# Optimization experiments

Hardware: AMD Instinct MI355X
Metric: run time of the kernel (lower is better)

The kernel has to match this reference:

```python
import jax, jax.numpy as jnp
import numpy as np
import math

B, S, D = 2, 1024, 1024
H, KVH = 16, 4
HD = D // H            # 64
WIN = 256              # sliding window size
E, TOPK = 8, 2
DFF = 4096
T = B * S
CAP = max(1, int(1.0 * T / E))   # capacity_factor=1.0 -> 256
EPS = 1e-6
NEG_INF = float('-inf')


def setup_inputs() -> dict:
    key = jax.random.key(0)
    ks = jax.random.split(key, 10)
    x = jax.random.normal(ks[0], (B, S, D), dtype=jnp.float32)
    # causal additive mask (B,1,S,S)
    i = jnp.arange(S)[:, None]
    j = jnp.arange(S)[None, :]
    causal = jnp.where(j <= i, 0.0, NEG_INF).astype(jnp.float32)
    mask = jnp.broadcast_to(causal[None, None], (B, 1, S, S))
    global_token_mask = jax.random.uniform(ks[1], (B, S)) < 0.05
    sd = 1.0 / math.sqrt(D)
    Wq = jax.random.normal(ks[2], (D, D), jnp.float32) * sd
    Wk = jax.random.normal(ks[3], (D, D), jnp.float32) * sd
    Wv = jax.random.normal(ks[4], (D, D), jnp.float32) * sd
    Wo = jax.random.normal(ks[5], (D, D), jnp.float32) * sd
    g1 = jnp.ones((D,), jnp.float32)
    g2 = jnp.ones((D,), jnp.float32)
    Wgate = jax.random.normal(ks[6], (D, E), jnp.float32) * 0.02
    W1 = jax.random.normal(ks[7], (E, D, 2 * DFF), jnp.float32) * sd
    W2 = jax.random.normal(ks[8], (E, DFF, D), jnp.float32) * (1.0 / math.sqrt(DFF))
    return {"x": x, "mask": mask, "global_token_mask": global_token_mask,
            "Wq": Wq, "Wk": Wk, "Wv": Wv, "Wo": Wo,
            "g1": g1, "g2": g2, "Wgate": Wgate, "W1": W1, "W2": W2}


def _rope_tables():
    inv_freq = 1.0 / (10000.0 ** (jnp.arange(0, HD, 2, dtype=jnp.float32) / HD))
    t = jnp.arange(S, dtype=jnp.float32)
    freqs = t[:, None] * inv_freq[None, :]          # (S, HD/2)
    emb = jnp.concatenate([freqs, freqs], axis=-1)  # (S, HD)
    return emb[None, None].astype(jnp.float32), None  # placeholder


def _rotate_half(x):
    x1, x2 = jnp.split(x, 2, axis=-1)
    return jnp.concatenate([-x2, x1], axis=-1)


def _rmsnorm(x, g):
    return g * x * jax.lax.rsqrt(jnp.mean(x * x, axis=-1, keepdims=True) + EPS)


def _attention(x, mask, gtm, Wq, Wk, Wv, Wo):
    # The torch GQA view/permute chain reduces exactly to a plain head split.
    q = (x @ Wq).reshape(B, S, H, HD).transpose(0, 2, 1, 3)  # (B,H,S,HD)
    k = (x @ Wk).reshape(B, S, H, HD).transpose(0, 2, 1, 3)
    v = (x @ Wv).reshape(B, S, H, HD).transpose(0, 2, 1, 3)
    # inline RoPE
    inv_freq = 1.0 / (10000.0 ** (jnp.arange(0, HD, 2, dtype=jnp.float32) / HD))
    t = jnp.arange(S, dtype=jnp.float32)
    freqs = t[:, None] * inv_freq[None, :]
    emb = jnp.concatenate([freqs, freqs], axis=-1)  # (S,HD)
    cos = jnp.cos(emb)[None, None]
    sin = jnp.sin(emb)[None, None]
    q = q * cos + _rotate_half(q) * sin
    k = k * cos + _rotate_half(k) * sin
    scores = jnp.einsum('bhqd,bhkd->bhqk', q, k) / math.sqrt(HD)
    # sliding-window mask
    i = jnp.arange(S)[:, None]
    j = jnp.arange(S)[None, :]
    diff = i - j
    swa = jnp.where((diff < 0) | (diff >= WIN), NEG_INF, 0.0).astype(scores.dtype)
    combined = mask + swa[None, None]               # (B,1,S,S)
    gt = gtm[:, None, :, None]                      # query is global
    gs = gtm[:, None, None, :]                      # key is global
    combined = jnp.where(gt | gs, 0.0, combined)
    attn = jax.nn.softmax(scores + combined, axis=-1)
    out = jnp.einsum('bhqk,bhkd->bhqd', attn, v)
    out = out.transpose(0, 2, 1, 3).reshape(B, S, D)
    return out @ Wo


def _moe(x, Wgate, W1, W2):
    flat_x = x.reshape(T, D)
    gate_scores = jax.nn.softmax(flat_x @ Wgate, axis=-1)          # (T,E)
    topk_vals, topk_idx = jax.lax.top_k(gate_scores, TOPK)          # (T,k)
    phi_mean = jnp.mean(gate_scores, axis=0)
    aux_loss = E * jnp.sum(phi_mean * phi_mean)
    # per-token weight for each expert (0 if not routed)
    w = jnp.zeros((T, E), flat_x.dtype).at[jnp.arange(T)[:, None], topk_idx].add(topk_vals)
    # capacity: pick top-CAP tokens by weight per expert. Unrouted tokens have
    # weight 0 so any that slip in contribute exactly 0 (matches torch semantics).
    sel_w, sel_idx = jax.lax.top_k(w.T, CAP)                        # (E,CAP)
    tok = flat_x[sel_idx]                                           # (E,CAP,D)
    h = jnp.einsum('ecd,edf->ecf', tok, W1)                         # (E,CAP,2*DFF)
    h1, h2 = jnp.split(h, 2, axis=-1)
    act = h1 * jax.nn.silu(h2)                                      # SwiGLU
    out_e = jnp.einsum('ecf,efd->ecd', act, W2) * sel_w[..., None]
    combined = jnp.zeros((T, D), flat_x.dtype).at[sel_idx.reshape(-1)].add(out_e.reshape(-1, D))
    return combined.reshape(B, S, D), aux_loss


def reference(x, mask, global_token_mask, Wq, Wk, Wv, Wo, g1, g2, Wgate, W1, W2):
    # pre-norm residual block (SublayerConnection with RMSNorm, dropout=identity in eval)
    h = x + _attention(_rmsnorm(x, g1), mask, global_token_mask, Wq, Wk, Wv, Wo)
    moe_out, aux_loss = _moe(_rmsnorm(h, g2), Wgate, W1, W2)
    out = h + moe_out
    return out, aux_loss
```

## Files before the change

### kernel.cpp

```cpp
#include <hip/hip_runtime.h>
#include <hip/hip_bf16.h>
#include <math.h>

#define T_TOK 2048
#define DMODEL 1024
#define NH 16
#define HD 64
#define S_LEN 1024
#define NE 8
#define CAP 256
#define DFF 4096

typedef __attribute__((ext_vector_type(8))) short bf16x8;
typedef __attribute__((ext_vector_type(4))) float f32x4;

__device__ inline unsigned short f2bf(float f) {
    union { float f; unsigned int u; } x; x.f = f;
    unsigned int u = x.u;
    unsigned int r = (u + 0x7FFFu + ((u >> 16) & 1u)) >> 16;
    return (unsigned short)r;
}

__device__ inline float bf2f(unsigned short h) {
    union { unsigned int u; float f; } x; x.u = (unsigned int)h << 16; return x.f;
}

__device__ inline unsigned int pkbf(float lo, float hi) {
    __hip_bfloat162 h2 = __float22bfloat162_rn(make_float2(lo, hi));
    unsigned int r;
    __builtin_memcpy(&r, &h2, 4);
    return r;
}

__device__ inline void gload16(const void* g, void* l) {
    __builtin_amdgcn_global_load_lds(
        (const __attribute__((address_space(1))) unsigned int*)g,
        (__attribute__((address_space(3))) unsigned int*)l, 16, 0, 0);
}

__global__ void rope_table_kernel(float* __restrict__ rc, float* __restrict__ rs) {
    int s = blockIdx.x;
    int i = threadIdx.x;
    float invf = powf(10000.0f, -(float)(2 * i) / 64.0f);
    float ang = (float)s * invf;
    rc[s * 32 + i] = cosf(ang);
    rs[s * 32 + i] = sinf(ang);
}

template <int OUTBF>
__global__ __launch_bounds__(256) void rmsnorm_kernel(const float* __restrict__ x,
                                                      const float* __restrict__ g,
                                                      void* __restrict__ yv) {
    __shared__ float red[256];
    int t = blockIdx.x;
    int tid = threadIdx.x;
    const float* xr = x + (size_t)t * DMODEL;
    float ss = 0.f;
    for (int d = tid; d < DMODEL; d += 256) { float v = xr[d]; ss += v * v; }
    red[tid] = ss; __syncthreads();
    for (int o = 128; o > 0; o >>= 1) { if (tid < o) red[tid] += red[tid + o]; __syncthreads(); }
    float scale = 1.0f / sqrtf(red[0] / (float)DMODEL + 1e-6f);
    if (OUTBF) {
        unsigned short* yr = (unsigned short*)yv + (size_t)t * DMODEL;
        for (int d = tid; d < DMODEL; d += 256) yr[d] = f2bf(g[d] * xr[d] * scale);
    } else {
        float* yr = (float*)yv + (size_t)t * DMODEL;
        for (int d = tid; d < DMODEL; d += 256) yr[d] = g[d] * xr[d] * scale;
    }
}

__global__ __launch_bounds__(256) void transpose_bf16(const float* __restrict__ src,
                                                      unsigned short* __restrict__ dst,
                                                      int ldS, int ldD,
                                                      long long sS, long long sD) {
    __shared__ float tile[64][65];
    src += (long long)blockIdx.z * sS;
    dst += (long long)blockIdx.z * sD;
    int c0 = blockIdx.x * 64, r0 = blockIdx.y * 64;
    int tr = threadIdx.x >> 4;
    int tc4 = (threadIdx.x & 15) * 4;
    #pragma unroll
    for (int j = 0; j < 4; j++) {
        float4 v = *(const float4*)&src[(size_t)(r0 + tr + j * 16) * ldS + c0 + tc4];
        tile[tr + j * 16][tc4 + 0] = v.x;
        tile[tr + j * 16][tc4 + 1] = v.y;
        tile[tr + j * 16][tc4 + 2] = v.z;
        tile[tr + j * 16][tc4 + 3] = v.w;
    }
    __syncthreads();
    int oc = threadIdx.x >> 3;
    int or8 = (threadIdx.x & 7) * 8;
    #pragma unroll
    for (int j = 0; j < 2; j++) {
        int c = oc + j * 32;
        unsigned short tmp[8];
        #pragma unroll
        for (int u = 0; u < 8; u++) tmp[u] = f2bf(tile[or8 + u][c]);
        *(uint4*)&dst[(size_t)(c0 + c) * ldD + r0 + or8] = *(uint4*)tmp;
    }
}

template <int BN, int RES>
__global__ __launch_bounds__(256) void gemm_mfma(const unsigned short* __restrict__ A,
                                                 const unsigned short* __restrict__ BT,
                                                 const float* __restrict__ Rr,
                                                 float* __restrict__ C,
                                                 int K, int lda, int ldc,
                                                 long long sA, long long sB, long long sC) {
    constexpr int BM = 128, BK = 64;
    constexpr int NF = BN / 32;
    __shared__ unsigned short As[BM * BK];
    __shared__ unsigned short Bs[BN * BK];
    A += (long long)blockIdx.z * sA;
    BT += (long long)blockIdx.z * sB;
    C += (long long)blockIdx.z * sC;
    const int tid = threadIdx.x;
    const int lane = tid & 63;
    const int wid = tid >> 6;
    const int wr = wid >> 1, wc = wid & 1;
    const int bx = blockIdx.x * BN, by = blockIdx.y * BM;

    f32x4 acc[4][NF] = {};

    for (int k0 = 0; k0 < K; k0 += BK) {
        #pragma unroll
        for (int i = 0; i < (BM * 8) / 256; i++) {
            int c = i * 256 + tid;
            int row = c >> 3, slot = c & 7;
            int gs = slot ^ (row & 7);
            gload16(A + (size_t)(by + row) * lda + k0 + gs * 8, &As[c * 8]);
        }
        #pragma unroll
        for (int i = 0; i < (BN * 8) / 256; i++) {
            int c = i * 256 + tid;
            int row = c >> 3, slot = c & 7;
            int gs = slot ^ (row & 7);
            gload16(BT + (size_t)(bx + row) * K + k0 + gs * 8, &Bs[c * 8]);
        }
        __syncthreads();
        #pragma unroll
        for (int ks = 0; ks < 2; ks++) {
            bf16x8 af[4], bfr[NF];
            #pragma unroll
            for (int m = 0; m < 4; m++) {
                int row = wr * 64 + m * 16 + (lane & 15);
                int slot = (ks * 4 + (lane >> 4)) ^ (row & 7);
                af[m] = *(const bf16x8*)&As[row * 64 + slot * 8];
            }
            #pragma unroll
            for (int n = 0; n < NF; n++) {
                int row = wc * (BN / 2) + n * 16 + (lane & 15);
                int slot = (ks * 4 + (lane >> 4)) ^ (row & 7);
                bfr[n] = *(const bf16x8*)&Bs[row * 64 + slot * 8];
            }
            #pragma unroll
            for (int m = 0; m < 4; m++)
                #pragma unroll
                for (int n = 0; n < NF; n++)
                    acc[m][n] = __builtin_amdgcn_mfma_f32_16x16x32_bf16(af[m], bfr[n], acc[m][n], 0, 0, 0);
        }
        __syncthreads();
    }
    #pragma unroll
    for (int m = 0; m < 4; m++) {
        int row0 = by + wr * 64 + m * 16 + (lane >> 4) * 4;
        #pragma unroll
        for (int n = 0; n < NF; n++) {
            int col = bx + wc * (BN / 2) + n * 16 + (lane & 15);
            #pragma unroll
            for (int r = 0; r < 4; r++) {
                size_t idx = (size_t)(row0 + r) * ldc + col;
                float v = acc[m][n][r];
                if (RES == 1) v += Rr[idx];
                if (RES == 2) v += C[idx];
                C[idx] = v;
            }
        }
    }
}

__global__ __launch_bounds__(256) void gemm_w1_fused(const unsigned short* __restrict__ tok,
                                                     const float* __restrict__ W1,
                                                     unsigned short* __restrict__ act) {
    __shared__ unsigned short As[256 * 64];
    __shared__ unsigned int B1p[32 * 32];
    __shared__ unsigned int B2p[32 * 32];
    const int e = blockIdx.y;
    const int bx = blockIdx.x * 32;
    const unsigned short* A = tok + (size_t)e * CAP * DMODEL;
    const float* B = W1 + (size_t)e * DMODEL * (2 * DFF);
    unsigned short* C = act + (size_t)e * CAP * DFF;
    const int tid = threadIdx.x, l = tid & 63, wid = tid >> 6;
    const int g = l >> 4;
    const int kp = tid >> 3;
    const int nc = tid & 7;
    const int chunk = kp >> 2, within = kp & 3;

    f32x4 acc1[4][2] = {};
    f32x4 acc2[4][2] = {};

    for (int k0 = 0; k0 < DMODEL; k0 += 64) {
        #pragma unroll
        for (int i = 0; i < 8; i++) {
            int c = i * 256 + tid;
            int row = c >> 3, sl = c & 7, gs = sl ^ (row & 7);
            gload16(A + (size_t)row * DMODEL + k0 + gs * 8, &As[c * 8]);
        }
        const float* Brow = B + (size_t)(k0 + 2 * kp) * 8192 + bx + nc * 4;
        float4 a0 = *(const float4*)(Brow);
        float4 a1 = *(const float4*)(Brow + 8192);
        float4 c0 = *(const float4*)(Brow + 4096);
        float4 c1 = *(const float4*)(Brow + 4096 + 8192);
        unsigned int p1[4], p2[4];
        p1[0] = pkbf(a0.x, a1.x); p1[1] = pkbf(a0.y, a1.y);
        p1[2] = pkbf(a0.z, a1.z); p1[3] = pkbf(a0.w, a1.w);
        p2[0] = pkbf(c0.x, c1.x); p2[1] = pkbf(c0.y, c1.y);
        p2[2] = pkbf(c0.z, c1.z); p2[3] = pkbf(c0.w, c1.w);
        #pragma unroll
        for (int i = 0; i < 4; i++) {
            int n_loc = nc * 4 + i;
            int idx = n_loc * 32 + ((chunk ^ (n_loc & 7)) << 2) + within;
            B1p[idx] = p1[i];
            B2p[idx] = p2[i];
        }
        __syncthreads();
        #pragma unroll
        for (int ks = 0; ks < 2; ks++) {
            bf16x8 af[4];
            #pragma unroll
            for (int m = 0; m < 4; m++) {
                int row = wid * 64 + m * 16 + (l & 15);
                int sl = (ks * 4 + g) ^ (row & 7);
                af[m] = *(const bf16x8*)&As[row * 64 + sl * 8];
            }
            #pragma unroll
            for (int nf = 0; nf < 2; nf++) {
                int n_loc = nf * 16 + (l & 15);
                int base = n_loc * 32 + (((ks * 4 + g) ^ (n_loc & 7)) << 2);
                bf16x8 b1 = *(const bf16x8*)&B1p[base];
                bf16x8 b2 = *(const bf16x8*)&B2p[base];
                #pragma unroll
                for (int m = 0; m < 4; m++) {
                    acc1[m][nf] = __builtin_amdgcn_mfma_f32_16x16x32_bf16(af[m], b1, acc1[m][nf], 0, 0, 0);
                    acc2[m][nf] = __builtin_amdgcn_mfma_f32_16x16x32_bf16(af[m], b2, acc2[m][nf], 0, 0, 0);
                }
            }
        }
        __syncthreads();
    }
    #pragma unroll
    for (int m = 0; m < 4; m++) {
        int row0 = wid * 64 + m * 16 + (l >> 4) * 4;
        #pragma unroll
        for (int nf = 0; nf < 2; nf++) {
            int col = bx + nf * 16 + (l & 15);
            #pragma unroll
            for (int r = 0; r < 4; r++) {
                float h1 = acc1[m][nf][r], h2 = acc2[m][nf][r];
                float sil = h2 / (1.0f + __expf(-h2));
                C[(size_t)(row0 + r) * DFF + col] = f2bf(h1 * sil);
            }
        }
    }
}

__global__ __launch_bounds__(256) void gemm_w2_fused(const unsigned short* __restrict__ act,
                                                     const float* __restrict__ W2,
                                                     float* __restrict__ oute) {
    __shared__ unsigned short As[128 * 64];
    __shared__ unsigned int Bp[32 * 32];
    const int e = blockIdx.y >> 1, mb = blockIdx.y & 1;
    const int bx = blockIdx.x * 32;
    const unsigned short* A = act + (size_t)e * CAP * DFF + (size_t)mb * 128 * DFF;
    const float* B = W2 + (size_t)e * DFF * DMODEL;
    float* C = oute + (size_t)e * CAP * DMODEL + (size_t)mb * 128 * DMODEL;
    const int tid = threadIdx.x, l = tid & 63, wid = tid >> 6;
    const int g = l >> 4;
    const int kp = tid >> 3;
    const int nc = tid & 7;
    const int chunk = kp >> 2, within = kp & 3;

    f32x4 acc[2][2] = {};

    for (int k0 = 0; k0 < DFF; k0 += 64) {
        #pragma unroll
        for (int i = 0; i < 4; i++) {
            int c = i * 256 + tid;
            int row = c >> 3, sl = c & 7, gs = sl ^ (row & 7);
            gload16(A + (size_t)row * DFF + k0 + gs * 8, &As[c * 8]);
        }
        const float* Brow = B + (size_t)(k0 + 2 * kp) * DMODEL + bx + nc * 4;
        float4 a0 = *(const float4*)(Brow);
        float4 a1 = *(const float4*)(Brow + DMODEL);
        unsigned int p1[4];
        p1[0] = pkbf(a0.x, a1.x); p1[1] = pkbf(a0.y, a1.y);
        p1[2] = pkbf(a0.z, a1.z); p1[3] = pkbf(a0.w, a1.w);
        #pragma unroll
        for (int i = 0; i < 4; i++) {
            int n_loc = nc * 4 + i;
            int idx = n_loc * 32 + ((chunk ^ (n_loc & 7)) << 2) + within;
            Bp[idx] = p1[i];
        }
        __syncthreads();
        #pragma unroll
        for (int ks = 0; ks < 2; ks++) {
            bf16x8 af[2];
            #pragma unroll
            for (int m = 0; m < 2; m++) {
                int row = wid * 32 + m * 16 + (l & 15);
                int sl = (ks * 4 + g) ^ (row & 7);
                af[m] = *(const bf16x8*)&As[row * 64 + sl * 8];
            }
            #pragma unroll
            for (int nf = 0; nf < 2; nf++) {
                int n_loc = nf * 16 + (l & 15);
                int base = n_loc * 32 + (((ks * 4 + g) ^ (n_loc & 7)) << 2);
                bf16x8 bfr = *(const bf16x8*)&Bp[base];
                #pragma unroll
                for (int m = 0; m < 2; m++)
                    acc[m][nf] = __builtin_amdgcn_mfma_f32_16x16x32_bf16(af[m], bfr, acc[m][nf], 0, 0, 0);
            }
        }
        __syncthreads();
    }
    #pragma unroll
    for (int m = 0; m < 2; m++) {
        int row0 = wid * 32 + m * 16 + (l >> 4) * 4;
        #pragma unroll
        for (int nf = 0; nf < 2; nf++) {
            int col = bx + nf * 16 + (l & 15);
            #pragma unroll
            for (int r = 0; r < 4; r++)
                C[(size_t)(row0 + r) * DMODEL + col] = acc[m][nf][r];
        }
    }
}

__global__ __launch_bounds__(512) void rope_cvt_kernel(const float* __restrict__ qkv,
                                                       const float* __restrict__ rc,
                                                       const float* __restrict__ rs,
                                                       unsigned short* __restrict__ Qh,
                                                       unsigned short* __restrict__ Ql,
                                                       unsigned short* __restrict__ Kh,
                                                       unsigned short* __restrict__ Kl) {
    int t = blockIdx.x;
    int b = t >> 10, s = t & 1023;
    int hh = threadIdx.x >> 5, i = threadIdx.x & 31;
    float c = rc[s * 32 + i], sn = rs[s * 32 + i];
    size_t base = (size_t)t * 3072 + hh * 64;
    float qa = qkv[base + i], qb_ = qkv[base + i + 32];
    float ka = qkv[base + 1024 + i], kb_ = qkv[base + 1024 + i + 32];
    size_t ob = ((size_t)(b * 16 + hh) * 1024 + s) * 64;
    float q0 = (qa * c - qb_ * sn) * 0.125f;
    float q1 = (qb_ * c + qa * sn) * 0.125f;
    float k0 = ka * c - kb_ * sn;
    float k1 = kb_ * c + ka * sn;
    unsigned short h0, h1;
    h0 = f2bf(q0); Qh[ob + i] = h0;      Ql[ob + i] = f2bf(q0 - bf2f(h0));
    h1 = f2bf(q1); Qh[ob + i + 32] = h1; Ql[ob + i + 32] = f2bf(q1 - bf2f(h1));
    h0 = f2bf(k0); Kh[ob + i] = h0;      Kl[ob + i] = f2bf(k0 - bf2f(h0));
    h1 = f2bf(k1); Kh[ob + i + 32] = h1; Kl[ob + i + 32] = f2bf(k1 - bf2f(h1));
}

__global__ __launch_bounds__(256) void vt_cvt_kernel(const float* __restrict__ qkv,
                                                     unsigned short* __restrict__ Vtb) {
    __shared__ float tile[32][65];
    int st = blockIdx.x;
    int bh = blockIdx.y;
    int b = bh >> 4, h = bh & 15;
    int tid = threadIdx.x;
    int s0 = st * 32;
    int sr = tid >> 3, c8 = (tid & 7) * 8;
    const float* src = qkv + (size_t)(b * 1024 + s0 + sr) * 3072 + 2048 + h * 64 + c8;
    #pragma unroll
    for (int u = 0; u < 8; u++) tile[sr][c8 + u] = src[u];
    __syncthreads();
    int d = tid & 63, sj = (tid >> 6) * 8;
    unsigned short tmp[8];
    #pragma unroll
    for (int u = 0; u < 8; u++) tmp[u] = f2bf(tile[sj + u][d]);
    *(uint4*)(Vtb + ((size_t)bh * 64 + d) * 1024 + s0 + sj) = *(uint4*)tmp;
}

__global__ __launch_bounds__(256) void attn_mfma_kernel(const unsigned short* __restrict__ Qh,
                                                        const unsigned short* __restrict__ Ql,
                                                        const unsigned short* __restrict__ Kh,
                                                        const unsigned short* __restrict__ Kl,
                                                        const unsigned short* __restrict__ Vtb,
                                                        const int* __restrict__ gtm,
                                                        unsigned short* __restrict__ o) {
    __shared__ unsigned short Ksh[64 * 64];
    __shared__ unsigned short Ksl[64 * 64];
    __shared__ unsigned short Vs[64 * 64];
    __shared__ unsigned short Pl[4][16 * 64];
    const int qt = blockIdx.x, h = blockIdx.y, b = blockIdx.z;
    const int bh = b * 16 + h;
    const int tid = threadIdx.x, l = tid & 63, w = tid >> 6;
    const int q0 = qt * 64 + w * 16;
    const unsigned short* Qhb = Qh + (size_t)bh * 1024 * 64;
    const unsigned short* Qlb = Ql + (size_t)bh * 1024 * 64;
    const unsigned short* Khb = Kh + (size_t)bh * 1024 * 64;
    const unsigned short* Klb = Kl + (size_t)bh * 1024 * 64;
    const unsigned short* Vbh = Vtb + (size_t)bh * 64 * 1024;
    const int* gb = gtm + b * 1024;

    bf16x8 afh[2], afl[2];
    #pragma unroll
    for (int ks = 0; ks < 2; ks++) {
        size_t off = (size_t)(q0 + (l & 15)) * 64 + ks * 32 + (l >> 4) * 8;
        afh[ks] = *(const bf16x8*)(Qhb + off);
        afl[ks] = *(const bf16x8*)(Qlb + off);
    }

    int gqm = 0;
    #pragma unroll
    for (int r = 0; r < 4; r++)
        gqm |= (gb[q0 + (l >> 4) * 4 + r] ? 1 : 0) << r;

    f32x4 acc_o[4] = {};
    float m_run[4], l_run[4];
    #pragma unroll
    for (int r = 0; r < 4; r++) { m_run[r] = -1e30f; l_run[r] = 0.f; }

    for (int jt = 0; jt < 16; jt++) {
        const int j0 = jt * 64;
        #pragma unroll
        for (int i = 0; i < 2; i++) {
            int c = i * 256 + tid, row = c >> 3, sl = c & 7, gs = sl ^ (row & 7);
            gload16(Khb + (size_t)(j0 + row) * 64 + gs * 8, &Ksh[c * 8]);
            gload16(Klb + (size_t)(j0 + row) * 64 + gs * 8, &Ksl[c * 8]);
            gload16(Vbh + (size_t)row * 1024 + j0 + gs * 8, &Vs[c * 8]);
        }
        __syncthreads();

        f32x4 sv[4] = {};
        #pragma unroll
        for (int n = 0; n < 4; n++) {
            #pragma unroll
            for (int ks = 0; ks < 2; ks++) {
                int row = n * 16 + (l & 15);
                int sl = (ks * 4 + (l >> 4)) ^ (row & 7);
                bf16x8 khf = *(const bf16x8*)&Ksh[row * 64 + sl * 8];
                bf16x8 klf = *(const bf16x8*)&Ksl[row * 64 + sl * 8];
                sv[n] = __builtin_amdgcn_mfma_f32_16x16x32_bf16(afl[ks], khf, sv[n], 0, 0, 0);
                sv[n] = __builtin_amdgcn_mfma_f32_16x16x32_bf16(afh[ks], klf, sv[n], 0, 0, 0);
                sv[n] = __builtin_amdgcn_mfma_f32_16x16x32_bf16(afh[ks], khf, sv[n], 0, 0, 0);
            }
        }

        int gk[4];
        #pragma unroll
        for (int n = 0; n < 4; n++) gk[n] = gb[j0 + n * 16 + (l & 15)];

        #pragma unroll
        for (int n = 0; n < 4; n++)
            #pragma unroll
            for (int r = 0; r < 4; r++) {
                int q = q0 + (l >> 4) * 4 + r;
                int k = j0 + n * 16 + (l & 15);
                bool allowed = ((gqm >> r) & 1) || gk[n] || ((k <= q) && (q - k < 256));
                if (!allowed) sv[n][r] = -1e30f;
            }

        {
            float tm[4], corr[4], rsum[4];
            #pragma unroll
            for (int r = 0; r < 4; r++)
                tm[r] = fmaxf(fmaxf(sv[0][r], sv[1][r]), fmaxf(sv[2][r], sv[3][r]));
            #pragma unroll
            for (int wd = 1; wd <= 8; wd <<= 1)
                #pragma unroll
                for (int r = 0; r < 4; r++) tm[r] = fmaxf(tm[r], __shfl_xor(tm[r], wd, 64));
            #pragma unroll
            for (int r = 0; r < 4; r++) {
                float mn = fmaxf(m_run[r], tm[r]);
                corr[r] = __expf(m_run[r] - mn);
                m_run[r] = mn;
                rsum[r] = 0.f;
            }
            #pragma unroll
            for (int n = 0; n < 4; n++)
                #pragma unroll
                for (int r = 0; r < 4; r++) {
                    float p = __expf(sv[n][r] - m_run[r]);
                    sv[n][r] = p;
                    rsum[r] += p;
                }
            #pragma unroll
            for (int wd = 1; wd <= 8; wd <<= 1)
                #pragma unroll
                for (int r = 0; r < 4; r++) rsum[r] += __shfl_xor(rsum[r], wd, 64);
            #pragma unroll
            for (int r = 0; r < 4; r++) l_run[r] = l_run[r] * corr[r] + rsum[r];
            #pragma unroll
            for (int nd = 0; nd < 4; nd++)
                #pragma unroll
                for (int r = 0; r < 4; r++) acc_o[nd][r] *= corr[r];
            #pragma unroll
            for (int n = 0; n < 4; n++)
                #pragma unroll
                for (int r = 0; r < 4; r++) {
                    int qr = (l >> 4) * 4 + r;
                    int kc = n * 16 + (l & 15);
                    int byte = (qr * 128 + kc * 2) ^ ((qr & 7) << 4);
                    Pl[w][byte >> 1] = f2bf(sv[n][r]);
                }
        }

        asm volatile("s_waitcnt lgkmcnt(0)" ::: "memory");
        __builtin_amdgcn_sched_barrier(0);

        #pragma unroll
        for (int ks = 0; ks < 2; ks++) {
            int prow = l & 15;
            int psl = (ks * 4 + (l >> 4)) ^ (prow & 7);
            bf16x8 pa = *(const bf16x8*)&Pl[w][prow * 64 + psl * 8];
            #pragma unroll
            for (int nd = 0; nd < 4; nd++) {
                int row = nd * 16 + (l & 15);
                int sl = (ks * 4 + (l >> 4)) ^ (row & 7);
                bf16x8 vf = *(const bf16x8*)&Vs[row * 64 + sl * 8];
                acc_o[nd] = __builtin_amdgcn_mfma_f32_16x16x32_bf16(pa, vf, acc_o[nd], 0, 0, 0);
            }
        }
        __syncthreads();
    }

    #pragma unroll
    for (int r = 0; r < 4; r++) {
        float inv = 1.0f / l_run[r];
        int t_ = b * 1024 + q0 + (l >> 4) * 4 + r;
        #pragma unroll
        for (int nd = 0; nd < 4; nd++) {
            int col = h * 64 + nd * 16 + (l & 15);
            o[(size_t)t_ * 1024 + col] = f2bf(acc_o[nd][r] * inv);
        }
    }
}

__global__ __launch_bounds__(256) void gate_kernel(const float* __restrict__ hn,
                                                   const float* __restrict__ Wgate,
                                                   float* __restrict__ wfull,
                                                   float* __restrict__ gate_sum) {
    int tid = threadIdx.x;
    int w = tid >> 6, l = tid & 63;
    int t = blockIdx.x * 4 + w;
    int e = l & 7, g = l >> 3;
    const float* xr = hn + (size_t)t * DMODEL;
    const float* wp = Wgate + l;
    float acc = 0.f;
    #pragma unroll 8
    for (int kk = 0; kk < 128; kk++)
        acc += xr[g + 8 * kk] * wp[64 * kk];
    #pragma unroll
    for (int o = 8; o < 64; o <<= 1) acc += __shfl_xor(acc, o, 64);
    float m = acc;
    #pragma unroll
    for (int o = 1; o < 8; o <<= 1) m = fmaxf(m, __shfl_xor(m, o, 64));
    float p = __expf(acc - m);
    float s = p;
    #pragma unroll
    for (int o = 1; o < 8; o <<= 1) s += __shfl_xor(s, o, 64);
    float pr = p / s;
    if (l < 8) atomicAdd(&gate_sum[e], pr);
    unsigned long long key = ((unsigned long long)__float_as_uint(pr) << 32) | (unsigned)(7 - e);
    unsigned long long k1 = key;
    #pragma unroll
    for (int o = 1; o < 8; o <<= 1) { unsigned long long t2 = __shfl_xor(k1, o, 64); if (t2 > k1) k1 = t2; }
    int e1 = 7 - (int)(k1 & 7);
    float v1 = __uint_as_float((unsigned)(k1 >> 32));
    unsigned long long key2 = (e == e1) ? 0ull : key;
    unsigned long long k2 = key2;
    #pragma unroll
    for (int o = 1; o < 8; o <<= 1) { unsigned long long t2 = __shfl_xor(k2, o, 64); if (t2 > k2) k2 = t2; }
    int e2 = 7 - (int)(k2 & 7);
    float v2 = __uint_as_float((unsigned)(k2 >> 32));
    if (l == 0) {
        wfull[t * 8 + e1] = v1;
        wfull[t * 8 + e2] = v2;
    }
}

__global__ __launch_bounds__(1024) void expert_select_kernel(const float* __restrict__ wfull,
                                                             float* __restrict__ sw,
                                                             int* __restrict__ sidx,
                                                             int* __restrict__ slot) {
    __shared__ unsigned long long keys[2048];
    int e = blockIdx.x;
    int t = threadIdx.x;
    for (int i = t; i < 2048; i += 1024) {
        float w = wfull[i * 8 + e];
        unsigned int wb = __float_as_uint(w);
        keys[i] = ((unsigned long long)wb << 32) | (unsigned long long)(0xFFFFFFFFu - (unsigned int)i);
    }
    __syncthreads();
    for (int k = 2; k <= 2048; k <<= 1) {
        for (int j = k >> 1; j > 0; j >>= 1) {
            for (int i = t; i < 2048; i += 1024) {
                int ixj = i ^ j;
                if (ixj > i) {
                    bool desc = ((i & k) == 0);
                    unsigned long long a = keys[i], b = keys[ixj];
                    if ((a < b) == desc) { keys[i] = b; keys[ixj] = a; }
                }
            }
            __syncthreads();
        }
    }
    if (t < CAP) {
        unsigned long long kk = keys[t];
        float w = __uint_as_float((unsigned int)(kk >> 32));
        int idx = (int)(0xFFFFFFFFu - (unsigned int)(kk & 0xFFFFFFFFu));
        sw[e * CAP + t] = w;
        sidx[e * CAP + t] = idx;
        if (w > 0.f) slot[idx * 8 + e] = t;
    }
}

__global__ __launch_bounds__(256) void gather_tok_kernel(const float* __restrict__ hn,
                                                         const int* __restrict__ sidx,
                                                         const float* __restrict__ sw,
                                                         unsigned short* __restrict__ tok) {
    int ec = blockIdx.x;
    int tid = threadIdx.x;
    float w = sw[ec];
    int src = sidx[ec];
    const float* s = hn + (size_t)src * DMODEL;
    unsigned short* d = tok + (size_t)ec * DMODEL;
    for (int i = tid; i < DMODEL; i += 256) d[i] = (w > 0.f) ? f2bf(s[i]) : 0;
}

__global__ __launch_bounds__(256) void combine_kernel(const float* __restrict__ h,
                                                      const float* __restrict__ out_e,
                                                      const int* __restrict__ slot,
                                                      const float* __restrict__ wfull,
                                                      const float* __restrict__ gate_sum,
                                                      float* __restrict__ out) {
    int t = blockIdx.x;
    int tid = threadIdx.x;
    for (int d = tid; d < DMODEL; d += 256) {
        float acc = h[(size_t)t * DMODEL + d];
        #pragma unroll
        for (int e = 0; e < 8; e++) {
            int c = slot[t * 8 + e];
            if (c >= 0) acc += wfull[t * 8 + e] * out_e[((size_t)(e * CAP + c)) * DMODEL + d];
        }
        out[(size_t)t * DMODEL + d] = acc;
    }
    if (t == 0 && tid == 0) {
        float a = 0.f;
        #pragma unroll
        for (int e = 0; e < 8; e++) { float m = gate_sum[e] / (float)T_TOK; a += m * m; }
        out[(size_t)T_TOK * DMODEL] = 8.0f * a;
    }
}

extern "C" void kernel_launch(void* const* d_in, const int* in_sizes, int n_in,
                              void* d_out, int out_size, void* d_ws, size_t ws_size,
                              hipStream_t stream) {
    const float* x     = (const float*)d_in[0];
    const int*   gtm   = (const int*)d_in[2];
    const float* Wq    = (const float*)d_in[3];
    const float* Wk    = (const float*)d_in[4];
    const float* Wv    = (const float*)d_in[5];
    const float* Wo    = (const float*)d_in[6];
    const float* g1    = (const float*)d_in[7];
    const float* g2    = (const float*)d_in[8];
    const float* Wgate = (const float*)d_in[9];
    const float* W1    = (const float*)d_in[10];
    const float* W2    = (const float*)d_in[11];
    float* out = (float*)d_out;

    char* ws = (char*)d_ws;
    unsigned short* Qh   = (unsigned short*)(ws + 0);
    unsigned short* Ql   = (unsigned short*)(ws + 4194304);
    unsigned short* Kh   = (unsigned short*)(ws + 8388608);
    unsigned short* Kl   = (unsigned short*)(ws + 12582912);
    unsigned short* Vtb  = (unsigned short*)(ws + 16777216);
    unsigned short* WqkvT = (unsigned short*)(ws + 33554432);
    unsigned short* WoT   = (unsigned short*)(ws + 39845888);
    unsigned short* xn    = (unsigned short*)(ws + 41943040);
    unsigned short* attno = (unsigned short*)(ws + 46137344);
    float* qkvb  = (float*)(ws + 50331648);
    float* oute  = (float*)(ws + 50331648);
    unsigned short* act = (unsigned short*)(ws + 33554432);
    float* hb    = (float*)(ws + 75497472);
    float* hnb   = (float*)(ws + 83886080);
    unsigned short* tok = (unsigned short*)(ws + 92274688);
    float* ropec = (float*)(ws + 96468992);
    float* ropes = (float*)(ws + 96600064);
    float* wfull = (float*)(ws + 96731136);
    int*   slot  = (int*)(ws + 96796672);
    float* sw    = (float*)(ws + 96862208);
    int*   sidx  = (int*)(ws + 96870400);
    float* gsum  = (float*)(ws + 96878592);

    rope_table_kernel<<<S_LEN, 32, 0, stream>>>(ropec, ropes);
    rmsnorm_kernel<1><<<T_TOK, 256, 0, stream>>>(x, g1, xn);

    transpose_bf16<<<dim3(16, 16, 1), 256, 0, stream>>>(Wq, WqkvT, 1024, 1024, 0, 0);
    transpose_bf16<<<dim3(16, 16, 1), 256, 0, stream>>>(Wk, WqkvT + 1024 * 1024, 1024, 1024, 0, 0);
    transpose_bf16<<<dim3(16, 16, 1), 256, 0, stream>>>(Wv, WqkvT + 2048 * 1024, 1024, 1024, 0, 0);
    transpose_bf16<<<dim3(16, 16, 1), 256, 0, stream>>>(Wo, WoT, 1024, 1024, 0, 0);

    gemm_mfma<128, 0><<<dim3(24, 16, 1), 256, 0, stream>>>(
        xn, WqkvT, nullptr, qkvb, 1024, 1024, 3072, 0, 0, 0);

    rope_cvt_kernel<<<T_TOK, 512, 0, stream>>>(qkvb, ropec, ropes, Qh, Ql, Kh, Kl);
    vt_cvt_kernel<<<dim3(32, 32, 1), 256, 0, stream>>>(qkvb, Vtb);

    attn_mfma_kernel<<<dim3(16, 16, 2), 256, 0, stream>>>(Qh, Ql, Kh, Kl, Vtb, gtm, attno);

    gemm_mfma<64, 1><<<dim3(16, 16, 1), 256, 0, stream>>>(
        attno, WoT, x, hb, 1024, 1024, 1024, 0, 0, 0);
    rmsnorm_kernel<0><<<T_TOK, 256, 0, stream>>>(hb, g2, hnb);

    hipMemsetAsync(wfull, 0, (size_t)T_TOK * NE * 4, stream);
    hipMemsetAsync(slot, 0xFF, (size_t)T_TOK * NE * 4, stream);
    hipMemsetAsync(gsum, 0, 8 * 4, stream);

    gate_kernel<<<T_TOK / 4, 256, 0, stream>>>(hnb, Wgate, wfull, gsum);
    expert_select_kernel<<<NE, 1024, 0, stream>>>(wfull, sw, sidx, slot);
    gather_tok_kernel<<<NE * CAP, 256, 0, stream>>>(hnb, sidx, sw, tok);

    gemm_w1_fused<<<dim3(128, 8, 1), 256, 0, stream>>>(tok, W1, act);
    gemm_w2_fused<<<dim3(32, 16, 1), 256, 0, stream>>>(act, W2, oute);

    combine_kernel<<<T_TOK, 256, 0, stream>>>(hb, oute, slot, wfull, gsum, out);
}
```

Before: 372.3 us.

## Fuse QKV projection with RoPE/V-transpose and drop weight transpose and memset launches

After: 356.4 us (median of 2 runs). 1.04x faster.

```diff
diff --git a/kernel.cpp b/kernel.cpp
--- a/kernel.cpp
+++ b/kernel.cpp
@@ -38,13 +38,15 @@
         (__attribute__((address_space(3))) unsigned int*)l, 16, 0, 0);
 }
 
-__global__ void rope_table_kernel(float* __restrict__ rc, float* __restrict__ rs) {
+__global__ void rope_table_kernel(float* __restrict__ rc, float* __restrict__ rs,
+                                  float* __restrict__ gsum) {
     int s = blockIdx.x;
     int i = threadIdx.x;
     float invf = powf(10000.0f, -(float)(2 * i) / 64.0f);
     float ang = (float)s * invf;
     rc[s * 32 + i] = cosf(ang);
     rs[s * 32 + i] = sinf(ang);
+    if (blockIdx.x == 0 && threadIdx.x < 8) gsum[threadIdx.x] = 0.f;
 }
 
 template <int OUTBF>
@@ -69,110 +71,191 @@
     }
 }
 
-__global__ __launch_bounds__(256) void transpose_bf16(const float* __restrict__ src,
-                                                      unsigned short* __restrict__ dst,
-                                                      int ldS, int ldD,
-                                                      long long sS, long long sD) {
-    __shared__ float tile[64][65];
-    src += (long long)blockIdx.z * sS;
-    dst += (long long)blockIdx.z * sD;
-    int c0 = blockIdx.x * 64, r0 = blockIdx.y * 64;
-    int tr = threadIdx.x >> 4;
-    int tc4 = (threadIdx.x & 15) * 4;
-    #pragma unroll
-    for (int j = 0; j < 4; j++) {
-        float4 v = *(const float4*)&src[(size_t)(r0 + tr + j * 16) * ldS + c0 + tc4];
-        tile[tr + j * 16][tc4 + 0] = v.x;
-        tile[tr + j * 16][tc4 + 1] = v.y;
-        tile[tr + j * 16][tc4 + 2] = v.z;
-        tile[tr + j * 16][tc4 + 3] = v.w;
-    }
-    __syncthreads();
-    int oc = threadIdx.x >> 3;
-    int or8 = (threadIdx.x & 7) * 8;
-    #pragma unroll
-    for (int j = 0; j < 2; j++) {
-        int c = oc + j * 32;
-        unsigned short tmp[8];
-        #pragma unroll
-        for (int u = 0; u < 8; u++) tmp[u] = f2bf(tile[or8 + u][c]);
-        *(uint4*)&dst[(size_t)(c0 + c) * ldD + r0 + or8] = *(uint4*)tmp;
-    }
-}
-
-template <int BN, int RES>
-__global__ __launch_bounds__(256) void gemm_mfma(const unsigned short* __restrict__ A,
-                                                 const unsigned short* __restrict__ BT,
+__global__ __launch_bounds__(256) void gemm_qkv_rope(const unsigned short* __restrict__ xn,
+                                                     const float* __restrict__ Wq,
+                                                     const float* __restrict__ Wk,
+                                                     const float* __restrict__ Wv,
+                                                     const float* __restrict__ rc,
+                                                     const float* __restrict__ rs,
+                                                     unsigned short* __restrict__ Qh,
+                                                     unsigned short* __restrict__ Ql,
+                                                     unsigned short* __restrict__ Kh,
+                                                     unsigned short* __restrict__ Kl,
+                                                     unsigned short* __restrict__ Vtb) {
+    __shared__ unsigned short As[128 * 64];
+    __shared__ unsigned int Bp[64 * 32];
+    const int mat = blockIdx.x >> 4;
+    const int h = blockIdx.x & 15;
+    const float* B = ((mat == 0) ? Wq : (mat == 1) ? Wk : Wv) + h * 64;
+    const int by = blockIdx.y * 128;
+    const int tid = threadIdx.x, l = tid & 63, wid = tid >> 6;
+    const int g = l >> 4;
+    const int kp = tid >> 3;
+    const int nc = tid & 7;
+    const int chunk = kp >> 2, within = kp & 3;
+
+    f32x4 acc[2][4] = {};
+
+    for (int k0 = 0; k0 < 1024; k0 += 64) {
+        #pragma unroll
+        for (int i = 0; i < 4; i++) {
+            int c = i * 256 + tid;
+            int row = c >> 3, sl = c & 7, gs = sl ^ (row & 7);
+            gload16(xn + (size_t)(by + row) * 1024 + k0 + gs * 8, &As[c * 8]);
+        }
+        const float* Brow = B + (size_t)(k0 + 2 * kp) * 1024 + nc * 8;
+        float4 a0 = *(const float4*)(Brow);
+        float4 a1 = *(const float4*)(Brow + 4);
+        float4 b0 = *(const float4*)(Brow + 1024);
+        float4 b1 = *(const float4*)(Brow + 1028);
+        unsigned int p[8];
+        p[0] = pkbf(a0.x, b0.x); p[1] = pkbf(a0.y, b0.y);
+        p[2] = pkbf(a0.z, b0.z); p[3] = pkbf(a0.w, b0.w);
+        p[4] = pkbf(a1.x, b1.x); p[5] = pkbf(a1.y, b1.y);
+        p[6] = pkbf(a1.z, b1.z); p[7] = pkbf(a1.w, b1.w);
+        #pragma unroll
+        for (int i = 0; i < 8; i++) {
+            int n_loc = nc * 8 + i;
+            int idx = n_loc * 32 + ((chunk ^ (n_loc & 7)) << 2) + within;
+            Bp[idx] = p[i];
+        }
+        __syncthreads();
+        #pragma unroll
+        for (int ks = 0; ks < 2; ks++) {
+            bf16x8 af[2];
+            #pragma unroll
+            for (int m = 0; m < 2; m++) {
+                int row = wid * 32 + m * 16 + (l & 15);
+                int sl = (ks * 4 + g) ^ (row & 7);
+                af[m] = *(const bf16x8*)&As[row * 64 + sl * 8];
+            }
+            #pragma unroll
+            for (int nf = 0; nf < 4; nf++) {
+                int n_loc = nf * 16 + (l & 15);
+                int base = n_loc * 32 + (((ks * 4 + g) ^ (n_loc & 7)) << 2);
+                bf16x8 bfr = *(const bf16x8*)&Bp[base];
+                #pragma unroll
+                for (int m = 0; m < 2; m++)
+                    acc[m][nf] = __builtin_amdgcn_mfma_f32_16x16x32_bf16(af[m], bfr, acc[m][nf], 0, 0, 0);
+            }
+        }
+        __syncthreads();
+    }
+
+    if (mat < 2) {
+        unsigned short* Dh = (mat == 0) ? Qh : Kh;
+        unsigned short* Dl = (mat == 0) ? Ql : Kl;
+        float scale = (mat == 0) ? 0.125f : 1.0f;
+        #pragma unroll
+        for (int m = 0; m < 2; m++)
+            #pragma unroll
+            for (int r = 0; r < 4; r++) {
+                int t = by + wid * 32 + m * 16 + g * 4 + r;
+                int b = t >> 10, s = t & 1023;
+                size_t ob = ((size_t)(b * 16 + h) * 1024 + s) * 64;
+                #pragma unroll
+                for (int pr = 0; pr < 2; pr++) {
+                    int i = pr * 16 + (l & 15);
+                    float c = rc[s * 32 + i], sn = rs[s * 32 + i];
+                    float a = acc[m][pr][r], bb = acc[m][pr + 2][r];
+                    float v0 = (a * c - bb * sn) * scale;
+                    float v1 = (bb * c + a * sn) * scale;
+                    unsigned short h0 = f2bf(v0), h1 = f2bf(v1);
+                    Dh[ob + i] = h0;      Dl[ob + i] = f2bf(v0 - bf2f(h0));
+                    Dh[ob + i + 32] = h1; Dl[ob + i + 32] = f2bf(v1 - bf2f(h1));
+                }
+            }
+    } else {
+        #pragma unroll
+        for (int m = 0; m < 2; m++) {
+            int t0 = by + wid * 32 + m * 16 + g * 4;
+            int b = t0 >> 10, s0 = t0 & 1023;
+            #pragma unroll
+            for (int nf = 0; nf < 4; nf++) {
+                int d = nf * 16 + (l & 15);
+                unsigned short tmp[4];
+                #pragma unroll
+                for (int r = 0; r < 4; r++) tmp[r] = f2bf(acc[m][nf][r]);
+                *(uint2*)&Vtb[((size_t)(b * 16 + h) * 64 + d) * 1024 + s0] = *(uint2*)tmp;
+            }
+        }
+    }
+}
+
+template <int RES>
+__global__ __launch_bounds__(256) void gemm_bf32(const unsigned short* __restrict__ A,
+                                                 const float* __restrict__ B,
                                                  const float* __restrict__ Rr,
                                                  float* __restrict__ C,
-                                                 int K, int lda, int ldc,
+                                                 int K, int lda,
                                                  long long sA, long long sB, long long sC) {
-    constexpr int BM = 128, BK = 64;
-    constexpr int NF = BN / 32;
-    __shared__ unsigned short As[BM * BK];
-    __shared__ unsigned short Bs[BN * BK];
-    A += (long long)blockIdx.z * sA;
-    BT += (long long)blockIdx.z * sB;
-    C += (long long)blockIdx.z * sC;
-    const int tid = threadIdx.x;
-    const int lane = tid & 63;
-    const int wid = tid >> 6;
-    const int wr = wid >> 1, wc = wid & 1;
-    const int bx = blockIdx.x * BN, by = blockIdx.y * BM;
-
-    f32x4 acc[4][NF] = {};
-
-    for (int k0 = 0; k0 < K; k0 += BK) {
-        #pragma unroll
-        for (int i = 0; i < (BM * 8) / 256; i++) {
+    __shared__ unsigned short As[128 * 64];
+    __shared__ unsigned int Bp[32 * 32];
+    A += (long long)blockIdx.z * sA + (long long)blockIdx.y * 128 * lda;
+    B += (long long)blockIdx.z * sB;
+    C += (long long)blockIdx.z * sC + (long long)blockIdx.y * 128 * 1024;
+    const float* Rp = RES ? (Rr + (long long)blockIdx.y * 128 * 1024) : nullptr;
+    const int bx = blockIdx.x * 32;
+    const int tid = threadIdx.x, l = tid & 63, wid = tid >> 6;
+    const int g = l >> 4;
+    const int kp = tid >> 3;
+    const int nc = tid & 7;
+    const int chunk = kp >> 2, within = kp & 3;
+
+    f32x4 acc[2][2] = {};
+
+    for (int k0 = 0; k0 < K; k0 += 64) {
+        #pragma unroll
+        for (int i = 0; i < 4; i++) {
             int c = i * 256 + tid;
-            int row = c >> 3, slot = c & 7;
-            int gs = slot ^ (row & 7);
-            gload16(A + (size_t)(by + row) * lda + k0 + gs * 8, &As[c * 8]);
-        }
-        #pragma unroll
-        for (int i = 0; i < (BN * 8) / 256; i++) {
-            int c = i * 256 + tid;
-            int row = c >> 3, slot = c & 7;
-            int gs = slot ^ (row & 7);
-            gload16(BT + (size_t)(bx + row) * K + k0 + gs * 8, &Bs[c * 8]);
+            int row = c >> 3, sl = c & 7, gs = sl ^ (row & 7);
+            gload16(A + (size_t)row * lda + k0 + gs * 8, &As[c * 8]);
+        }
+        const float* Brow = B + (size_t)(k0 + 2 * kp) * 1024 + bx + nc * 4;
+        float4 a0 = *(const float4*)(Brow);
+        float4 a1 = *(const float4*)(Brow + 1024);
+        unsigned int p1[4];
+        p1[0] = pkbf(a0.x, a1.x); p1[1] = pkbf(a0.y, a1.y);
+        p1[2] = pkbf(a0.z, a1.z); p1[3] = pkbf(a0.w, a1.w);
+        #pragma unroll
+        for (int i = 0; i < 4; i++) {
+            int n_loc = nc * 4 + i;
+            int idx = n_loc * 32 + ((chunk ^ (n_loc & 7)) << 2) + within;
+            Bp[idx] = p1[i];
         }
         __syncthreads();
         #pragma unroll
         for (int ks = 0; ks < 2; ks++) {
-            bf16x8 af[4], bfr[NF];
-            #pragma unroll
-            for (int m = 0; m < 4; m++) {
-                int row = wr * 64 + m * 16 + (lane & 15);
-                int slot = (ks * 4 + (lane >> 4)) ^ (row & 7);
-                af[m] = *(const bf16x8*)&As[row * 64 + slot * 8];
-            }
-            #pragma unroll
-            for (int n = 0; n < NF; n++) {
-                int row = wc * (BN / 2) + n * 16 + (lane & 15);
-                int slot = (ks * 4 + (lane >> 4)) ^ (row & 7);
-                bfr[n] = *(const bf16x8*)&Bs[row * 64 + slot * 8];
-            }
-            #pragma unroll
-            for (int m = 0; m < 4; m++)
-                #pragma unroll
-                for (int n = 0; n < NF; n++)
-                    acc[m][n] = __builtin_amdgcn_mfma_f32_16x16x32_bf16(af[m], bfr[n], acc[m][n], 0, 0, 0);
-        }
-        __syncthreads();
-    }
-    #pragma unroll
-    for (int m = 0; m < 4; m++) {
-        int row0 = by + wr * 64 + m * 16 + (lane >> 4) * 4;
-        #pragma unroll
-        for (int n = 0; n < NF; n++) {
-            int col = bx + wc * (BN / 2) + n * 16 + (lane & 15);
+            bf16x8 af[2];
+            #pragma unroll
+            for (int m = 0; m < 2; m++) {
+                int row = wid * 32 + m * 16 + (l & 15);
+                int sl = (ks * 4 + g) ^ (row & 7);
+                af[m] = *(const bf16x8*)&As[row * 64 + sl * 8];
+            }
+            #pragma unroll
+            for (int nf = 0; nf < 2; nf++) {
+                int n_loc = nf * 16 + (l & 15);
+                int base = n_loc * 32 + (((ks * 4 + g) ^ (n_loc & 7)) << 2);
+                bf16x8 bfr = *(const bf16x8*)&Bp[base];
+                #pragma unroll
+                for (int m = 0; m < 2; m++)
+                    acc[m][nf] = __builtin_amdgcn_mfma_f32_16x16x32_bf16(af[m], bfr, acc[m][nf], 0, 0, 0);
+            }
+        }
+        __syncthreads();
+    }
+    #pragma unroll
+    for (int m = 0; m < 2; m++) {
+        int row0 = wid * 32 + m * 16 + g * 4;
+        #pragma unroll
+        for (int nf = 0; nf < 2; nf++) {
+            int col = bx + nf * 16 + (l & 15);
             #pragma unroll
             for (int r = 0; r < 4; r++) {
-                size_t idx = (size_t)(row0 + r) * ldc + col;
-                float v = acc[m][n][r];
-                if (RES == 1) v += Rr[idx];
-                if (RES == 2) v += C[idx];
+                size_t idx = (size_t)(row0 + r) * 1024 + col;
+                float v = acc[m][nf][r];
+                if (RES) v += Rp[idx];
                 C[idx] = v;
             }
         }
@@ -250,7 +333,7 @@
     }
     #pragma unroll
     for (int m = 0; m < 4; m++) {
-        int row0 = wid * 64 + m * 16 + (l >> 4) * 4;
+        int row0 = wid * 64 + m * 16 + g * 4;
         #pragma unroll
         for (int nf = 0; nf < 2; nf++) {
             int col = bx + nf * 16 + (l & 15);
@@ -262,124 +345,6 @@
             }
         }
     }
-}
-
-__global__ __launch_bounds__(256) void gemm_w2_fused(const unsigned short* __restrict__ act,
-                                                     const float* __restrict__ W2,
-                                                     float* __restrict__ oute) {
-    __shared__ unsigned short As[128 * 64];
-    __shared__ unsigned int Bp[32 * 32];
-    const int e = blockIdx.y >> 1, mb = blockIdx.y & 1;
-    const int bx = blockIdx.x * 32;
-    const unsigned short* A = act + (size_t)e * CAP * DFF + (size_t)mb * 128 * DFF;
-    const float* B = W2 + (size_t)e * DFF * DMODEL;
-    float* C = oute + (size_t)e * CAP * DMODEL + (size_t)mb * 128 * DMODEL;
-    const int tid = threadIdx.x, l = tid & 63, wid = tid >> 6;
-    const int g = l >> 4;
-    const int kp = tid >> 3;
-    const int nc = tid & 7;
-    const int chunk = kp >> 2, within = kp & 3;
-
-    f32x4 acc[2][2] = {};
-
-    for (int k0 = 0; k0 < DFF; k0 += 64) {
-        #pragma unroll
-        for (int i = 0; i < 4; i++) {
-            int c = i * 256 + tid;
-            int row = c >> 3, sl = c & 7, gs = sl ^ (row & 7);
-            gload16(A + (size_t)row * DFF + k0 + gs * 8, &As[c * 8]);
-        }
-        const float* Brow = B + (size_t)(k0 + 2 * kp) * DMODEL + bx + nc * 4;
-        float4 a0 = *(const float4*)(Brow);
-        float4 a1 = *(const float4*)(Brow + DMODEL);
-        unsigned int p1[4];
-        p1[0] = pkbf(a0.x, a1.x); p1[1] = pkbf(a0.y, a1.y);
-        p1[2] = pkbf(a0.z, a1.z); p1[3] = pkbf(a0.w, a1.w);
-        #pragma unroll
-        for (int i = 0; i < 4; i++) {
-            int n_loc = nc * 4 + i;
-            int idx = n_loc * 32 + ((chunk ^ (n_loc & 7)) << 2) + within;
-            Bp[idx] = p1[i];
-        }
-        __syncthreads();
-        #pragma unroll
-        for (int ks = 0; ks < 2; ks++) {
-            bf16x8 af[2];
-            #pragma unroll
-            for (int m = 0; m < 2; m++) {
-                int row = wid * 32 + m * 16 + (l & 15);
-                int sl = (ks * 4 + g) ^ (row & 7);
-                af[m] = *(const bf16x8*)&As[row * 64 + sl * 8];
-            }
-            #pragma unroll
-            for (int nf = 0; nf < 2; nf++) {
-                int n_loc = nf * 16 + (l & 15);
-                int base = n_loc * 32 + (((ks * 4 + g) ^ (n_loc & 7)) << 2);
-                bf16x8 bfr = *(const bf16x8*)&Bp[base];
-                #pragma unroll
-                for (int m = 0; m < 2; m++)
-                    acc[m][nf] = __builtin_amdgcn_mfma_f32_16x16x32_bf16(af[m], bfr, acc[m][nf], 0, 0, 0);
-            }
-        }
-        __syncthreads();
-    }
-    #pragma unroll
-    for (int m = 0; m < 2; m++) {
-        int row0 = wid * 32 + m * 16 + (l >> 4) * 4;
-        #pragma unroll
-        for (int nf = 0; nf < 2; nf++) {
-            int col = bx + nf * 16 + (l & 15);
-            #pragma unroll
-            for (int r = 0; r < 4; r++)
-                C[(size_t)(row0 + r) * DMODEL + col] = acc[m][nf][r];
-        }
-    }
-}
-
-__global__ __launch_bounds__(512) void rope_cvt_kernel(const float* __restrict__ qkv,
-                                                       const float* __restrict__ rc,
-                                                       const float* __restrict__ rs,
-                                                       unsigned short* __restrict__ Qh,
-                                                       unsigned short* __restrict__ Ql,
-                                                       unsigned short* __restrict__ Kh,
-                                                       unsigned short* __restrict__ Kl) {
-    int t = blockIdx.x;
-    int b = t >> 10, s = t & 1023;
-    int hh = threadIdx.x >> 5, i = threadIdx.x & 31;
-    float c = rc[s * 32 + i], sn = rs[s * 32 + i];
-    size_t base = (size_t)t * 3072 + hh * 64;
-    float qa = qkv[base + i], qb_ = qkv[base + i + 32];
-    float ka = qkv[base + 1024 + i], kb_ = qkv[base + 1024 + i + 32];
-    size_t ob = ((size_t)(b * 16 + hh) * 1024 + s) * 64;
-    float q0 = (qa * c - qb_ * sn) * 0.125f;
-    float q1 = (qb_ * c + qa * sn) * 0.125f;
-    float k0 = ka * c - kb_ * sn;
-    float k1 = kb_ * c + ka * sn;
-    unsigned short h0, h1;
-    h0 = f2bf(q0); Qh[ob + i] = h0;      Ql[ob + i] = f2bf(q0 - bf2f(h0));
-    h1 = f2bf(q1); Qh[ob + i + 32] = h1; Ql[ob + i + 32] = f2bf(q1 - bf2f(h1));
-    h0 = f2bf(k0); Kh[ob + i] = h0;      Kl[ob + i] = f2bf(k0 - bf2f(h0));
-    h1 = f2bf(k1); Kh[ob + i + 32] = h1; Kl[ob + i + 32] = f2bf(k1 - bf2f(h1));
-}
-
-__global__ __launch_bounds__(256) void vt_cvt_kernel(const float* __restrict__ qkv,
-                                                     unsigned short* __restrict__ Vtb) {
-    __shared__ float tile[32][65];
-    int st = blockIdx.x;
-    int bh = blockIdx.y;
-    int b = bh >> 4, h = bh & 15;
-    int tid = threadIdx.x;
-    int s0 = st * 32;
-    int sr = tid >> 3, c8 = (tid & 7) * 8;
-    const float* src = qkv + (size_t)(b * 1024 + s0 + sr) * 3072 + 2048 + h * 64 + c8;
-    #pragma unroll
-    for (int u = 0; u < 8; u++) tile[sr][c8 + u] = src[u];
-    __syncthreads();
-    int d = tid & 63, sj = (tid >> 6) * 8;
-    unsigned short tmp[8];
-    #pragma unroll
-    for (int u = 0; u < 8; u++) tmp[u] = f2bf(tile[sj + u][d]);
-    *(uint4*)(Vtb + ((size_t)bh * 64 + d) * 1024 + s0 + sj) = *(uint4*)tmp;
 }
 
 __global__ __launch_bounds__(256) void attn_mfma_kernel(const unsigned short* __restrict__ Qh,
@@ -541,6 +506,7 @@
 __global__ __launch_bounds__(256) void gate_kernel(const float* __restrict__ hn,
                                                    const float* __restrict__ Wgate,
                                                    float* __restrict__ wfull,
+                                                   int* __restrict__ slot,
                                                    float* __restrict__ gate_sum) {
     int tid = threadIdx.x;
     int w = tid >> 6, l = tid & 63;
@@ -562,22 +528,20 @@
     #pragma unroll
     for (int o = 1; o < 8; o <<= 1) s += __shfl_xor(s, o, 64);
     float pr = p / s;
-    if (l < 8) atomicAdd(&gate_sum[e], pr);
     unsigned long long key = ((unsigned long long)__float_as_uint(pr) << 32) | (unsigned)(7 - e);
     unsigned long long k1 = key;
     #pragma unroll
     for (int o = 1; o < 8; o <<= 1) { unsigned long long t2 = __shfl_xor(k1, o, 64); if (t2 > k1) k1 = t2; }
     int e1 = 7 - (int)(k1 & 7);
-    float v1 = __uint_as_float((unsigned)(k1 >> 32));
     unsigned long long key2 = (e == e1) ? 0ull : key;
     unsigned long long k2 = key2;
     #pragma unroll
     for (int o = 1; o < 8; o <<= 1) { unsigned long long t2 = __shfl_xor(k2, o, 64); if (t2 > k2) k2 = t2; }
     int e2 = 7 - (int)(k2 & 7);
-    float v2 = __uint_as_float((unsigned)(k2 >> 32));
-    if (l == 0) {
-        wfull[t * 8 + e1] = v1;
-        wfull[t * 8 + e2] = v2;
+    if (l < 8) {
+        wfull[t * 8 + e] = (e == e1 || e == e2) ? pr : 0.f;
+        slot[t * 8 + e] = -1;
+        atomicAdd(&gate_sum[e], pr);
     }
 }
 
@@ -677,54 +641,41 @@
     unsigned short* Kh   = (unsigned short*)(ws + 8388608);
     unsigned short* Kl   = (unsigned short*)(ws + 12582912);
     unsigned short* Vtb  = (unsigned short*)(ws + 16777216);
-    unsigned short* WqkvT = (unsigned short*)(ws + 33554432);
-    unsigned short* WoT   = (unsigned short*)(ws + 39845888);
-    unsigned short* xn    = (unsigned short*)(ws + 41943040);
-    unsigned short* attno = (unsigned short*)(ws + 46137344);
-    float* qkvb  = (float*)(ws + 50331648);
-    float* oute  = (float*)(ws + 50331648);
-    unsigned short* act = (unsigned short*)(ws + 33554432);
-    float* hb    = (float*)(ws + 75497472);
-    float* hnb   = (float*)(ws + 83886080);
-    unsigned short* tok = (unsigned short*)(ws + 92274688);
-    float* ropec = (float*)(ws + 96468992);
-    float* ropes = (float*)(ws + 96600064);
-    float* wfull = (float*)(ws + 96731136);
-    int*   slot  = (int*)(ws + 96796672);
-    float* sw    = (float*)(ws + 96862208);
-    int*   sidx  = (int*)(ws + 96870400);
-    float* gsum  = (float*)(ws + 96878592);
-
-    rope_table_kernel<<<S_LEN, 32, 0, stream>>>(ropec, ropes);
+    unsigned short* act  = (unsigned short*)(ws + 0);
+    unsigned short* xn   = (unsigned short*)(ws + 20971520);
+    unsigned short* attno= (unsigned short*)(ws + 25165824);
+    float* hb    = (float*)(ws + 29360128);
+    float* hnb   = (float*)(ws + 37748736);
+    float* oute  = (float*)(ws + 46137344);
+    unsigned short* tok = (unsigned short*)(ws + 54525952);
+    float* ropec = (float*)(ws + 58720256);
+    float* ropes = (float*)(ws + 58851328);
+    float* wfull = (float*)(ws + 58982400);
+    int*   slot  = (int*)(ws + 59047936);
+    float* sw    = (float*)(ws + 59113472);
+    int*   sidx  = (int*)(ws + 59121664);
+    float* gsum  = (float*)(ws + 59129856);
+
+    rope_table_kernel<<<S_LEN, 32, 0, stream>>>(ropec, ropes, gsum);
     rmsnorm_kernel<1><<<T_TOK, 256, 0, stream>>>(x, g1, xn);
 
-    transpose_bf16<<<dim3(16, 16, 1), 256, 0, stream>>>(Wq, WqkvT, 1024, 1024, 0, 0);
-    transpose_bf16<<<dim3(16, 16, 1), 256, 0, stream>>>(Wk, WqkvT + 1024 * 1024, 1024, 1024, 0, 0);
-    transpose_bf16<<<dim3(16, 16, 1), 256, 0, stream>>>(Wv, WqkvT + 2048 * 1024, 1024, 1024, 0, 0);
-    transpose_bf16<<<dim3(16, 16, 1), 256, 0, stream>>>(Wo, WoT, 1024, 1024, 0, 0);
-
-    gemm_mfma<128, 0><<<dim3(24, 16, 1), 256, 0, stream>>>(
-        xn, WqkvT, nullptr, qkvb, 1024, 1024, 3072, 0, 0, 0);
-
-    rope_cvt_kernel<<<T_TOK, 512, 0, stream>>>(qkvb, ropec, ropes, Qh, Ql, Kh, Kl);
-    vt_cvt_kernel<<<dim3(32, 32, 1), 256, 0, stream>>>(qkvb, Vtb);
+    gemm_qkv_rope<<<dim3(48, 16, 1), 256, 0, stream>>>(
+        xn, Wq, Wk, Wv, ropec, ropes, Qh, Ql, Kh, Kl, Vtb);
 
     attn_mfma_kernel<<<dim3(16, 16, 2), 256, 0, stream>>>(Qh, Ql, Kh, Kl, Vtb, gtm, attno);
 
-    gemm_mfma<64, 1><<<dim3(16, 16, 1), 256, 0, stream>>>(
-        attno, WoT, x, hb, 1024, 1024, 1024, 0, 0, 0);
+    gemm_bf32<1><<<dim3(32, 16, 1), 256, 0, stream>>>(
+        attno, Wo, x, hb, 1024, 1024, 0, 0, 0);
     rmsnorm_kernel<0><<<T_TOK, 256, 0, stream>>>(hb, g2, hnb);
 
-    hipMemsetAsync(wfull, 0, (size_t)T_TOK * NE * 4, stream);
-    hipMemsetAsync(slot, 0xFF, (size_t)T_TOK * NE * 4, stream);
-    hipMemsetAsync(gsum, 0, 8 * 4, stream);
-
-    gate_kernel<<<T_TOK / 4, 256, 0, stream>>>(hnb, Wgate, wfull, gsum);
+    gate_kernel<<<T_TOK / 4, 256, 0, stream>>>(hnb, Wgate, wfull, slot, gsum);
     expert_select_kernel<<<NE, 1024, 0, stream>>>(wfull, sw, sidx, slot);
     gather_tok_kernel<<<NE * CAP, 256, 0, stream>>>(hnb, sidx, sw, tok);
 
     gemm_w1_fused<<<dim3(128, 8, 1), 256, 0, stream>>>(tok, W1, act);
-    gemm_w2_fused<<<dim3(32, 16, 1), 256, 0, stream>>>(act, W2, oute);
+    gemm_bf32<0><<<dim3(32, 2, 8), 256, 0, stream>>>(
+        act, W2, nullptr, oute, 4096, 4096,
+        (long long)CAP * DFF, (long long)DFF * 1024, (long long)CAP * 1024);
 
     combine_kernel<<<T_TOK, 256, 0, stream>>>(hb, oute, slot, wfull, gsum, out);
 }
```
